# Performance work log

Hardware: AMD Instinct MI355X
Metric: run time of the kernel (lower is better)

Reference implementation:

```python
import jax, jax.numpy as jnp
import numpy as np

B, S, D = 2, 2048, 1024
H, DK = 16, 64  # num_heads, key_dim (value_dim defaults to key_dim)


def setup_inputs() -> dict:
    key = jax.random.key(0)
    ks = jax.random.split(key, 11)
    init = lambda k, shape, fan_in: jax.random.uniform(
        k, shape, jnp.float32, -1.0, 1.0) * (1.0 / np.sqrt(fan_in))
    return {
        "query": jax.random.normal(ks[0], (B, S, D), jnp.float32),
        "key": jax.random.normal(ks[1], (B, S, D), jnp.float32),
        "value": jax.random.normal(ks[2], (B, S, D), jnp.float32),
        "Wq": init(ks[3], (D, H, DK), D),
        "bq": jnp.zeros((H, DK), jnp.float32),
        "Wk": init(ks[4], (D, H, DK), D),
        "bk": jnp.zeros((H, DK), jnp.float32),
        "Wv": init(ks[5], (D, H, DK), D),
        "bv": jnp.zeros((H, DK), jnp.float32),
        "Wo": init(ks[6], (H, DK, D), H * DK),
        "bo": jnp.zeros((D,), jnp.float32),
    }


def reference(query, key, value, Wq, bq, Wk, bk, Wv, bv, Wo, bo):
    # QKV projections: abc,cde->abde (EinsumDense with bias on (H, DK))
    q = jnp.einsum("bsd,dhk->bshk", query, Wq) + bq  # [B,S,H,DK]
    k = jnp.einsum("bsd,dhk->bshk", key, Wk) + bk
    v = jnp.einsum("bsd,dhk->bshk", value, Wv) + bv
    # Keras scales the query before the dot product
    q = q * (1.0 / jnp.sqrt(jnp.asarray(DK, q.dtype)))
    # aecd,abcd->acbe : [B,H,Sq,Sk]
    scores = jnp.einsum("bqhk,bshk->bhqs", q, k)
    probs = jax.nn.softmax(scores, axis=-1)
    # acbe,aecd->abcd : [B,Sq,H,DK]
    attn = jnp.einsum("bhqs,bshk->bqhk", probs, v)
    # output projection: abcd,cde->abe
    out = jnp.einsum("bqhk,hkd->bqd", attn, Wo) + bo  # [B,S,D]
    return out
```

## Files before the change

### kernel.cpp

```cpp
#include <hip/hip_runtime.h>
#include <hip/hip_bf16.h>
#include <stdint.h>
#include <stddef.h>


typedef __bf16 bf16;
typedef __attribute__((ext_vector_type(4))) bf16 bf16x4;
typedef __attribute__((ext_vector_type(8))) bf16 bf16x8;
typedef __attribute__((ext_vector_type(4))) float f32x4;
typedef __attribute__((ext_vector_type(16))) float f32x16;
typedef __attribute__((ext_vector_type(2))) unsigned int uint2v;

#define DEVINL static __device__ __forceinline__

DEVINL void gload_lds16(const void* g, void* l) {
  __builtin_amdgcn_global_load_lds(
      (const __attribute__((address_space(1))) void*)g,
      (__attribute__((address_space(3))) void*)l, 16, 0, 0);
}

DEVINL f32x4 mfma16(bf16x8 a, bf16x8 b, f32x4 c) {
  return __builtin_amdgcn_mfma_f32_16x16x32_bf16(a, b, c, 0, 0, 0);
}
DEVINL f32x16 mfma32(bf16x8 a, bf16x8 b, f32x16 c) {
  return __builtin_amdgcn_mfma_f32_32x32x16_bf16(a, b, c, 0, 0, 0);
}
DEVINL unsigned pack2(float lo, float hi) {
  union { bf16 h[2]; unsigned u; } t;
  t.h[0] = (bf16)lo; t.h[1] = (bf16)hi;
  return t.u;
}
DEVINL bf16x8 mk8(unsigned a, unsigned b, unsigned c, unsigned d) {
  union { unsigned u[4]; bf16x8 v; } t;
  t.u[0] = a; t.u[1] = b; t.u[2] = c; t.u[3] = d;
  return t.v;
}

__global__ __launch_bounds__(256) void wt_kernel(
    const float* __restrict__ w0, const float* __restrict__ w1,
    const float* __restrict__ w2, const float* __restrict__ w3,
    bf16* __restrict__ out) {
  __shared__ float tile[64 * 65];
  int t = blockIdx.y;
  const float* w = (t == 0) ? w0 : (t == 1) ? w1 : (t == 2) ? w2 : w3;
  bf16* o = out + (size_t)t * 1024 * 1024;
  int tb = blockIdx.x;
  int k0 = (tb >> 4) * 64, n0 = (tb & 15) * 64;
  int c = threadIdx.x & 63, r0 = threadIdx.x >> 6;
  for (int r = r0; r < 64; r += 4)
    tile[r * 65 + c] = w[(size_t)(k0 + r) * 1024 + n0 + c];
  __syncthreads();
  for (int r = r0; r < 64; r += 4)
    o[(size_t)(n0 + r) * 1024 + k0 + c] = (bf16)tile[c * 65 + r];
}

__global__ __launch_bounds__(256) void gemm_qkv(
    const float* __restrict__ Aq, const float* __restrict__ Ak,
    const float* __restrict__ Av, const bf16* __restrict__ Wt,
    const float* __restrict__ bq, const float* __restrict__ bk,
    const float* __restrict__ bv,
    bf16* __restrict__ outQ, bf16* __restrict__ outK, bf16* __restrict__ Vt) {
  int z = blockIdx.z;
  const float* A   = (z == 0) ? Aq : (z == 1) ? Ak : Av;
  const bf16* Wz   = Wt + (size_t)z * 1024 * 1024;
  const float* bia = (z == 0) ? bq : (z == 1) ? bk : bv;
  float scale      = (z == 0) ? 0.125f : 1.0f;

  __shared__ bf16 As[128 * 32];
  __shared__ bf16 Bs[128 * 32];

  int m0 = blockIdx.x * 128, n0 = blockIdx.y * 128;
  int tid = threadIdx.x, w = tid >> 6, l = tid & 63;
  int wm = (w >> 1) * 64, wn = (w & 1) * 64;
  int c16 = l & 15, g = l >> 4;
  int ar = tid >> 1, akb = (tid & 1) * 16;

  f32x4 acc[4][4] = {};

  for (int kt = 0; kt < 1024; kt += 32) {
    for (int i = 0; i < 2; ++i) {
      int n = (w * 2 + i) * 16 + (l >> 2);
      int k = (l & 3) * 8;
      gload_lds16(Wz + (size_t)(n0 + n) * 1024 + kt + k,
                  (char*)Bs + (w * 2 + i) * 1024 + l * 16);
    }
    {
      const float* ap = A + (size_t)(m0 + ar) * 1024 + kt + akb;
      f32x4 f0 = *(const f32x4*)(ap + 0);
      f32x4 f1 = *(const f32x4*)(ap + 4);
      f32x4 f2 = *(const f32x4*)(ap + 8);
      f32x4 f3 = *(const f32x4*)(ap + 12);
      bf16x8 h0, h1;
#pragma unroll
      for (int j = 0; j < 4; ++j) {
        h0[j] = (bf16)f0[j]; h0[4 + j] = (bf16)f1[j];
        h1[j] = (bf16)f2[j]; h1[4 + j] = (bf16)f3[j];
      }
      *(bf16x8*)&As[ar * 32 + akb]     = h0;
      *(bf16x8*)&As[ar * 32 + akb + 8] = h1;
    }
    __syncthreads();
    bf16x8 af[4], bfr[4];
#pragma unroll
    for (int mt = 0; mt < 4; ++mt)
      af[mt] = *(const bf16x8*)&As[(wm + mt * 16 + c16) * 32 + g * 8];
#pragma unroll
    for (int nt = 0; nt < 4; ++nt)
      bfr[nt] = *(const bf16x8*)&Bs[(wn + nt * 16 + c16) * 32 + g * 8];
#pragma unroll
    for (int mt = 0; mt < 4; ++mt)
#pragma unroll
      for (int nt = 0; nt < 4; ++nt)
        acc[mt][nt] = mfma16(af[mt], bfr[nt], acc[mt][nt]);
    __syncthreads();
  }

  if (z < 2) {
    bf16* Cout = (z == 0) ? outQ : outK;
#pragma unroll
    for (int mt = 0; mt < 4; ++mt)
#pragma unroll
      for (int nt = 0; nt < 4; ++nt) {
        int n = n0 + wn + nt * 16 + c16;
        float bb = bia[n];
#pragma unroll
        for (int r = 0; r < 4; ++r) {
          int m = m0 + wm + mt * 16 + g * 4 + r;
          Cout[(size_t)m * 1024 + n] = (bf16)((acc[mt][nt][r] + bb) * scale);
        }
      }
  } else {
#pragma unroll
    for (int mt = 0; mt < 4; ++mt)
#pragma unroll
      for (int nt = 0; nt < 4; ++nt) {
        int n = n0 + wn + nt * 16 + c16;
        float bb = bia[n];
        int m = m0 + wm + mt * 16 + g * 4;
        int b = m >> 11, s = m & 2047;
        bf16x4 v;
#pragma unroll
        for (int r = 0; r < 4; ++r) v[r] = (bf16)(acc[mt][nt][r] + bb);
        *(bf16x4*)&Vt[((size_t)(b * 16 + (n >> 6)) * 64 + (n & 63)) * 2048 + s] = v;
      }
  }
}

__global__ __launch_bounds__(256) void flash_kernel(
    const bf16* __restrict__ Qp, const bf16* __restrict__ Kp,
    const bf16* __restrict__ Vt, bf16* __restrict__ AO) {
  __shared__ __align__(16) bf16 Ks[2][64 * 64];
  __shared__ __align__(16) bf16 Vs[2][64 * 64];

  int orig = blockIdx.x;
  int wg = (orig & 7) * 64 + (orig >> 3);
  int bh = wg >> 4, qb = wg & 15;
  int b = bh >> 4, h = bh & 15;
  int tid = threadIdx.x, w = tid >> 6, l = tid & 63;
  int lo5 = l & 31, g = l >> 5;
  int q0 = qb * 128 + w * 32;

  const bf16* qptr = Qp + (size_t)(b * 2048 + q0 + lo5) * 1024 + h * 64 + g * 8;
  bf16x8 qf0 = *(const bf16x8*)(qptr + 0);
  bf16x8 qf1 = *(const bf16x8*)(qptr + 16);
  bf16x8 qf2 = *(const bf16x8*)(qptr + 32);
  bf16x8 qf3 = *(const bf16x8*)(qptr + 48);

  const bf16* kbase = Kp + (size_t)(b * 2048) * 1024 + h * 64;
  const bf16* vbase = Vt + (size_t)bh * 64 * 2048;

  int u0 = w * 64 + l;
  int u1 = (4 + w) * 64 + l;
  int r0s = u0 >> 3, c0s = (u0 & 7) ^ (r0s & 7);
  int r1s = u1 >> 3, c1s = (u1 & 7) ^ (r1s & 7);

#define STAGE(buf, s0)                                                          \
  do {                                                                          \
    gload_lds16(kbase + (size_t)((s0) + r0s) * 1024 + c0s * 8,                  \
                (bf16*)Ks[buf] + u0 * 8);                                       \
    gload_lds16(kbase + (size_t)((s0) + r1s) * 1024 + c1s * 8,                  \
                (bf16*)Ks[buf] + u1 * 8);                                       \
    gload_lds16(vbase + (size_t)r0s * 2048 + (s0) + c0s * 8,                    \
                (bf16*)Vs[buf] + u0 * 8);                                       \
    gload_lds16(vbase + (size_t)r1s * 2048 + (s0) + c1s * 8,                    \
                (bf16*)Vs[buf] + u1 * 8);                                       \
  } while (0)

#define LDSK(cp, nt, kt) \
  (*(const bf16x8*)&cp[(((nt)*32 + lo5) << 6) + (((((kt)*2 + g)) ^ (lo5 & 7)) << 3)])
#define LDSV(cp, dt, st) \
  (*(const bf16x8*)&cp[(((dt)*32 + lo5) << 6) + (((((st)*2 + g)) ^ (lo5 & 7)) << 3)])

  f32x16 o0 = {}, o1 = {};
  float ps0 = 0.f, ps1 = 0.f, ps2 = 0.f, ps3 = 0.f;

  STAGE(0, 0);
  int cur = 0;
  for (int t = 0; t < 32; ++t) {
    if (t < 31) {
      STAGE(cur ^ 1, (t + 1) * 64);
      asm volatile("s_waitcnt vmcnt(4)" ::: "memory");
    } else {
      asm volatile("s_waitcnt vmcnt(0)" ::: "memory");
    }
    __builtin_amdgcn_s_barrier();
    __builtin_amdgcn_sched_barrier(0);
    const bf16* kc = Ks[cur];
    const bf16* vc = Vs[cur];

    f32x16 sv = {};
    sv = mfma32(LDSK(kc, 0, 0), qf0, sv);
    sv = mfma32(LDSK(kc, 0, 1), qf1, sv);
    sv = mfma32(LDSK(kc, 0, 2), qf2, sv);
    sv = mfma32(LDSK(kc, 0, 3), qf3, sv);
    float p[16];
#pragma unroll
    for (int r = 0; r < 16; ++r) p[r] = __expf(sv[r]);
    ps0 += p[0] + p[4] + p[8] + p[12];
    ps1 += p[1] + p[5] + p[9] + p[13];
    ps2 += p[2] + p[6] + p[10] + p[14];
    ps3 += p[3] + p[7] + p[11] + p[15];
    unsigned pw0 = pack2(p[0], p[1]), pw1 = pack2(p[2], p[3]);
    unsigned pw2 = pack2(p[4], p[5]), pw3 = pack2(p[6], p[7]);
    unsigned pw4 = pack2(p[8], p[9]), pw5 = pack2(p[10], p[11]);
    unsigned pw6 = pack2(p[12], p[13]), pw7 = pack2(p[14], p[15]);
    uint2v a02 = __builtin_amdgcn_permlane32_swap(pw0, pw2, false, false);
    uint2v a13 = __builtin_amdgcn_permlane32_swap(pw1, pw3, false, false);
    uint2v a46 = __builtin_amdgcn_permlane32_swap(pw4, pw6, false, false);
    uint2v a57 = __builtin_amdgcn_permlane32_swap(pw5, pw7, false, false);
    bf16x8 pa0 = mk8(a02.x, a13.x, a02.y, a13.y);
    bf16x8 pa1 = mk8(a46.x, a57.x, a46.y, a57.y);

    f32x16 sw = {};
    sw = mfma32(LDSK(kc, 1, 0), qf0, sw);
    sw = mfma32(LDSK(kc, 1, 1), qf1, sw);
    sw = mfma32(LDSK(kc, 1, 2), qf2, sw);
    sw = mfma32(LDSK(kc, 1, 3), qf3, sw);
#pragma unroll
    for (int r = 0; r < 16; ++r) p[r] = __expf(sw[r]);
    ps0 += p[0] + p[4] + p[8] + p[12];
    ps1 += p[1] + p[5] + p[9] + p[13];
    ps2 += p[2] + p[6] + p[10] + p[14];
    ps3 += p[3] + p[7] + p[11] + p[15];
    pw0 = pack2(p[0], p[1]); pw1 = pack2(p[2], p[3]);
    pw2 = pack2(p[4], p[5]); pw3 = pack2(p[6], p[7]);
    pw4 = pack2(p[8], p[9]); pw5 = pack2(p[10], p[11]);
    pw6 = pack2(p[12], p[13]); pw7 = pack2(p[14], p[15]);
    a02 = __builtin_amdgcn_permlane32_swap(pw0, pw2, false, false);
    a13 = __builtin_amdgcn_permlane32_swap(pw1, pw3, false, false);
    a46 = __builtin_amdgcn_permlane32_swap(pw4, pw6, false, false);
    a57 = __builtin_amdgcn_permlane32_swap(pw5, pw7, false, false);
    bf16x8 pb0 = mk8(a02.x, a13.x, a02.y, a13.y);
    bf16x8 pb1 = mk8(a46.x, a57.x, a46.y, a57.y);

    o0 = mfma32(pa0, LDSV(vc, 0, 0), o0);
    o1 = mfma32(pa0, LDSV(vc, 1, 0), o1);
    o0 = mfma32(pa1, LDSV(vc, 0, 1), o0);
    o1 = mfma32(pa1, LDSV(vc, 1, 1), o1);
    o0 = mfma32(pb0, LDSV(vc, 0, 2), o0);
    o1 = mfma32(pb0, LDSV(vc, 1, 2), o1);
    o0 = mfma32(pb1, LDSV(vc, 0, 3), o0);
    o1 = mfma32(pb1, LDSV(vc, 1, 3), o1);

    __builtin_amdgcn_sched_barrier(0);
    __builtin_amdgcn_s_barrier();
    cur ^= 1;
  }
#undef STAGE
#undef LDSK
#undef LDSV

  float plsum = (ps0 + ps1) + (ps2 + ps3);
  float tot = plsum + __shfl_xor(plsum, 32);

#pragma unroll
  for (int r = 0; r < 16; ++r) {
    int qr = (r & 3) + 8 * (r >> 2) + 4 * g;
    float inv = 1.0f / __shfl(tot, qr);
    bf16* op = AO + (size_t)(b * 2048 + q0 + qr) * 1024 + h * 64 + lo5;
    op[0]  = (bf16)(o0[r] * inv);
    op[32] = (bf16)(o1[r] * inv);
  }
}

__global__ __launch_bounds__(256) void gemm_o(
    const bf16* __restrict__ A, const bf16* __restrict__ Wt3,
    const float* __restrict__ bo, float* __restrict__ C) {
  __shared__ bf16 As[128 * 32];
  __shared__ bf16 Bs[128 * 32];
  int m0 = blockIdx.x * 128, n0 = blockIdx.y * 128;
  int tid = threadIdx.x, w = tid >> 6, l = tid & 63;
  int wm = (w >> 1) * 64, wn = (w & 1) * 64;
  int c16 = l & 15, g = l >> 4;

  f32x4 acc[4][4] = {};
  for (int kt = 0; kt < 1024; kt += 32) {
    for (int i = 0; i < 2; ++i) {
      int rr = (w * 2 + i) * 16 + (l >> 2);
      int k = (l & 3) * 8;
      gload_lds16(A + (size_t)(m0 + rr) * 1024 + kt + k,
                  (char*)As + (w * 2 + i) * 1024 + l * 16);
      gload_lds16(Wt3 + (size_t)(n0 + rr) * 1024 + kt + k,
                  (char*)Bs + (w * 2 + i) * 1024 + l * 16);
    }
    __syncthreads();
    bf16x8 af[4], bfr[4];
#pragma unroll
    for (int mt = 0; mt < 4; ++mt)
      af[mt] = *(const bf16x8*)&As[(wm + mt * 16 + c16) * 32 + g * 8];
#pragma unroll
    for (int nt = 0; nt < 4; ++nt)
      bfr[nt] = *(const bf16x8*)&Bs[(wn + nt * 16 + c16) * 32 + g * 8];
#pragma unroll
    for (int mt = 0; mt < 4; ++mt)
#pragma unroll
      for (int nt = 0; nt < 4; ++nt)
        acc[mt][nt] = mfma16(af[mt], bfr[nt], acc[mt][nt]);
    __syncthreads();
  }
#pragma unroll
  for (int mt = 0; mt < 4; ++mt)
#pragma unroll
    for (int nt = 0; nt < 4; ++nt) {
      int n = n0 + wn + nt * 16 + c16;
      float bb = bo[n];
#pragma unroll
      for (int r = 0; r < 4; ++r) {
        int m = m0 + wm + mt * 16 + g * 4 + r;
        C[(size_t)m * 1024 + n] = acc[mt][nt][r] + bb;
      }
    }
}

extern "C" void kernel_launch(void* const* d_in, const int* in_sizes, int n_in,
                              void* d_out, int out_size, void* d_ws, size_t ws_size,
                              hipStream_t stream) {
  const float* query = (const float*)d_in[0];
  const float* key_  = (const float*)d_in[1];
  const float* value = (const float*)d_in[2];
  const float* Wq = (const float*)d_in[3];
  const float* bq = (const float*)d_in[4];
  const float* Wk = (const float*)d_in[5];
  const float* bk = (const float*)d_in[6];
  const float* Wv = (const float*)d_in[7];
  const float* bv = (const float*)d_in[8];
  const float* Wo = (const float*)d_in[9];
  const float* bo = (const float*)d_in[10];
  float* out = (float*)d_out;

  char* ws = (char*)d_ws;
  const size_t MB = 1024 * 1024;
  bf16* Wt = (bf16*)(ws);
  bf16* Qp = (bf16*)(ws + 8 * MB);
  bf16* Kp = (bf16*)(ws + 16 * MB);
  bf16* Vt = (bf16*)(ws + 24 * MB);
  bf16* AO = (bf16*)(ws + 32 * MB);

  dim3 blk(256);
  wt_kernel<<<dim3(256, 4), blk, 0, stream>>>(Wq, Wk, Wv, Wo, Wt);
  gemm_qkv<<<dim3(32, 8, 3), blk, 0, stream>>>(query, key_, value, Wt,
                                               bq, bk, bv, Qp, Kp, Vt);
  flash_kernel<<<dim3(512), blk, 0, stream>>>(Qp, Kp, Vt, AO);
  gemm_o<<<dim3(32, 8), blk, 0, stream>>>(AO, Wt + (size_t)3 * 1024 * 1024, bo, out);
}
```

Measured before the change: 136.9 us.

## Double-buffer LDS tiles and XOR-swizzle layout in QKV and output GEMMs

Both the QKV projection GEMM and the output projection GEMM now use two LDS buffers. The next K-tile is prefetched (global-to-LDS loads, plus fp32 A loads held in registers) while MFMAs run on the current tile, which removes one barrier per iteration. An XOR swizzle on the 16-byte k-chunks is applied on both the LDS writes and the LDS fragment reads to cut bank conflicts. This doubles LDS use per block and keeps the prefetched A values live in registers, which may lower occupancy.

Result: faster. 129.5 us (-5.4%).

```diff
diff --git a/kernel.cpp b/kernel.cpp
--- a/kernel.cpp
+++ b/kernel.cpp
@@ -66,54 +66,85 @@
   const float* bia = (z == 0) ? bq : (z == 1) ? bk : bv;
   float scale      = (z == 0) ? 0.125f : 1.0f;
 
-  __shared__ bf16 As[128 * 32];
-  __shared__ bf16 Bs[128 * 32];
+  __shared__ bf16 As[2][128 * 32];
+  __shared__ bf16 Bs[2][128 * 32];
 
   int m0 = blockIdx.x * 128, n0 = blockIdx.y * 128;
   int tid = threadIdx.x, w = tid >> 6, l = tid & 63;
   int wm = (w >> 1) * 64, wn = (w & 1) * 64;
   int c16 = l & 15, g = l >> 4;
+  int rsw = (c16 >> 1) & 3;
   int ar = tid >> 1, akb = (tid & 1) * 16;
+  int asw = (ar >> 1) & 3;
+  int as0 = (((akb >> 3) + 0) ^ asw) * 8;
+  int as1 = (((akb >> 3) + 1) ^ asw) * 8;
+
+  int brow0 = (w * 2 + 0) * 16 + (l >> 2);
+  int brow1 = (w * 2 + 1) * 16 + (l >> 2);
+  int bk0 = ((l & 3) ^ ((brow0 >> 1) & 3)) * 8;
+  int bk1 = ((l & 3) ^ ((brow1 >> 1) & 3)) * 8;
 
   f32x4 acc[4][4] = {};
 
+#define STAGE_B(buf, kt)                                                     \
+  do {                                                                       \
+    gload_lds16(Wz + (size_t)(n0 + brow0) * 1024 + (kt) + bk0,               \
+                (char*)Bs[buf] + (w * 2 + 0) * 1024 + l * 16);               \
+    gload_lds16(Wz + (size_t)(n0 + brow1) * 1024 + (kt) + bk1,               \
+                (char*)Bs[buf] + (w * 2 + 1) * 1024 + l * 16);               \
+  } while (0)
+
+#define PACK_A(buf)                                                          \
+  do {                                                                       \
+    bf16x8 h0, h1;                                                           \
+    _Pragma("unroll") for (int j = 0; j < 4; ++j) {                          \
+      h0[j] = (bf16)f0[j]; h0[4 + j] = (bf16)f1[j];                          \
+      h1[j] = (bf16)f2[j]; h1[4 + j] = (bf16)f3[j];                          \
+    }                                                                        \
+    *(bf16x8*)&As[buf][ar * 32 + as0] = h0;                                  \
+    *(bf16x8*)&As[buf][ar * 32 + as1] = h1;                                  \
+  } while (0)
+
+  STAGE_B(0, 0);
+  {
+    const float* ap = A + (size_t)(m0 + ar) * 1024 + akb;
+    f32x4 f0 = *(const f32x4*)(ap + 0);
+    f32x4 f1 = *(const f32x4*)(ap + 4);
+    f32x4 f2 = *(const f32x4*)(ap + 8);
+    f32x4 f3 = *(const f32x4*)(ap + 12);
+    PACK_A(0);
+  }
+  __syncthreads();
+
+  int cur = 0;
   for (int kt = 0; kt < 1024; kt += 32) {
-    for (int i = 0; i < 2; ++i) {
-      int n = (w * 2 + i) * 16 + (l >> 2);
-      int k = (l & 3) * 8;
-      gload_lds16(Wz + (size_t)(n0 + n) * 1024 + kt + k,
-                  (char*)Bs + (w * 2 + i) * 1024 + l * 16);
+    f32x4 f0, f1, f2, f3;
+    if (kt < 992) {
+      STAGE_B(cur ^ 1, kt + 32);
+      const float* ap = A + (size_t)(m0 + ar) * 1024 + kt + 32 + akb;
+      f0 = *(const f32x4*)(ap + 0);
+      f1 = *(const f32x4*)(ap + 4);
+      f2 = *(const f32x4*)(ap + 8);
+      f3 = *(const f32x4*)(ap + 12);
     }
-    {
-      const float* ap = A + (size_t)(m0 + ar) * 1024 + kt + akb;
-      f32x4 f0 = *(const f32x4*)(ap + 0);
-      f32x4 f1 = *(const f32x4*)(ap + 4);
-      f32x4 f2 = *(const f32x4*)(ap + 8);
-      f32x4 f3 = *(const f32x4*)(ap + 12);
-      bf16x8 h0, h1;
-#pragma unroll
-      for (int j = 0; j < 4; ++j) {
-        h0[j] = (bf16)f0[j]; h0[4 + j] = (bf16)f1[j];
-        h1[j] = (bf16)f2[j]; h1[4 + j] = (bf16)f3[j];
-      }
-      *(bf16x8*)&As[ar * 32 + akb]     = h0;
-      *(bf16x8*)&As[ar * 32 + akb + 8] = h1;
-    }
-    __syncthreads();
     bf16x8 af[4], bfr[4];
 #pragma unroll
     for (int mt = 0; mt < 4; ++mt)
-      af[mt] = *(const bf16x8*)&As[(wm + mt * 16 + c16) * 32 + g * 8];
+      af[mt] = *(const bf16x8*)&As[cur][(wm + mt * 16 + c16) * 32 + ((g ^ rsw) * 8)];
 #pragma unroll
     for (int nt = 0; nt < 4; ++nt)
-      bfr[nt] = *(const bf16x8*)&Bs[(wn + nt * 16 + c16) * 32 + g * 8];
+      bfr[nt] = *(const bf16x8*)&Bs[cur][(wn + nt * 16 + c16) * 32 + ((g ^ rsw) * 8)];
 #pragma unroll
     for (int mt = 0; mt < 4; ++mt)
 #pragma unroll
       for (int nt = 0; nt < 4; ++nt)
         acc[mt][nt] = mfma16(af[mt], bfr[nt], acc[mt][nt]);
+    if (kt < 992) PACK_A(cur ^ 1);
     __syncthreads();
-  }
+    cur ^= 1;
+  }
+#undef STAGE_B
+#undef PACK_A
 
   if (z < 2) {
     bf16* Cout = (z == 0) ? outQ : outK;
@@ -286,38 +317,56 @@
 __global__ __launch_bounds__(256) void gemm_o(
     const bf16* __restrict__ A, const bf16* __restrict__ Wt3,
     const float* __restrict__ bo, float* __restrict__ C) {
-  __shared__ bf16 As[128 * 32];
-  __shared__ bf16 Bs[128 * 32];
+  __shared__ bf16 As[2][128 * 32];
+  __shared__ bf16 Bs[2][128 * 32];
   int m0 = blockIdx.x * 128, n0 = blockIdx.y * 128;
   int tid = threadIdx.x, w = tid >> 6, l = tid & 63;
   int wm = (w >> 1) * 64, wn = (w & 1) * 64;
   int c16 = l & 15, g = l >> 4;
+  int rsw = (c16 >> 1) & 3;
+
+  int brow0 = (w * 2 + 0) * 16 + (l >> 2);
+  int brow1 = (w * 2 + 1) * 16 + (l >> 2);
+  int bk0 = ((l & 3) ^ ((brow0 >> 1) & 3)) * 8;
+  int bk1 = ((l & 3) ^ ((brow1 >> 1) & 3)) * 8;
 
   f32x4 acc[4][4] = {};
+
+#define STAGE_O(buf, kt)                                                     \
+  do {                                                                       \
+    gload_lds16(A + (size_t)(m0 + brow0) * 1024 + (kt) + bk0,                \
+                (char*)As[buf] + (w * 2 + 0) * 1024 + l * 16);               \
+    gload_lds16(A + (size_t)(m0 + brow1) * 1024 + (kt) + bk1,                \
+                (char*)As[buf] + (w * 2 + 1) * 1024 + l * 16);               \
+    gload_lds16(Wt3 + (size_t)(n0 + brow0) * 1024 + (kt) + bk0,              \
+                (char*)Bs[buf] + (w * 2 + 0) * 1024 + l * 16);               \
+    gload_lds16(Wt3 + (size_t)(n0 + brow1) * 1024 + (kt) + bk1,              \
+                (char*)Bs[buf] + (w * 2 + 1) * 1024 + l * 16);               \
+  } while (0)
+
+  STAGE_O(0, 0);
+  __syncthreads();
+
+  int cur = 0;
   for (int kt = 0; kt < 1024; kt += 32) {
-    for (int i = 0; i < 2; ++i) {
-      int rr = (w * 2 + i) * 16 + (l >> 2);
-      int k = (l & 3) * 8;
-      gload_lds16(A + (size_t)(m0 + rr) * 1024 + kt + k,
-                  (char*)As + (w * 2 + i) * 1024 + l * 16);
-      gload_lds16(Wt3 + (size_t)(n0 + rr) * 1024 + kt + k,
-                  (char*)Bs + (w * 2 + i) * 1024 + l * 16);
-    }
-    __syncthreads();
+    if (kt < 992) STAGE_O(cur ^ 1, kt + 32);
     bf16x8 af[4], bfr[4];
 #pragma unroll
     for (int mt = 0; mt < 4; ++mt)
-      af[mt] = *(const bf16x8*)&As[(wm + mt * 16 + c16) * 32 + g * 8];
+      af[mt] = *(const bf16x8*)&As[cur][(wm + mt * 16 + c16) * 32 + ((g ^ rsw) * 8)];
 #pragma unroll
     for (int nt = 0; nt < 4; ++nt)
-      bfr[nt] = *(const bf16x8*)&Bs[(wn + nt * 16 + c16) * 32 + g * 8];
+      bfr[nt] = *(const bf16x8*)&Bs[cur][(wn + nt * 16 + c16) * 32 + ((g ^ rsw) * 8)];
 #pragma unroll
     for (int mt = 0; mt < 4; ++mt)
 #pragma unroll
       for (int nt = 0; nt < 4; ++nt)
         acc[mt][nt] = mfma16(af[mt], bfr[nt], acc[mt][nt]);
     __syncthreads();
-  }
+    cur ^= 1;
+  }
+#undef STAGE_O
+
 #pragma unroll
   for (int mt = 0; mt < 4; ++mt)
 #pragma unroll
```
